# Optimization experiments

Hardware: AMD Instinct MI355X
Metric: run time of the kernel (lower is better)

## Reference

```python
import jax, jax.numpy as jnp
import numpy as np

IN_ = 64
FEATURE = 1024
BATCH = 256

def setup_inputs() -> dict:
    key = jax.random.key(0)
    kx, kw = jax.random.split(key)
    x = jax.random.normal(kx, (BATCH, IN_, FEATURE), dtype=jnp.float32)
    # W[i] corresponds to torch Linear weight of shape [out_features, in_features]
    # scaled like torch's default kaiming-uniform-ish init (bound = 1/sqrt(fan_in))
    bound = 1.0 / np.sqrt(FEATURE)
    W = jax.random.uniform(kw, (IN_, FEATURE, FEATURE), dtype=jnp.float32,
                           minval=-bound, maxval=bound)
    return {"x": x, "W": W}

def reference(x, W):
    # Per-position independent linear: out[b,i,o] = sum_f x[b,i,f] * W[i,o,f]
    # (torch Linear computes x @ W^T). Single batched GEMM via einsum.
    return jnp.einsum('bif,iof->bio', x, W)
```

## Files before the change

### kernel.cpp

```cpp
#include <hip/hip_runtime.h>
#include <hip/hip_bf16.h>

#define IN_CNT 64
#define FEAT   1024
#define BATCH  256

#define BM 256
#define BN 256
#define BK 64
#define KT (FEAT / BK)

typedef __attribute__((ext_vector_type(4))) float f32x4;
typedef __attribute__((ext_vector_type(4))) short bf16x4;
typedef __attribute__((ext_vector_type(8))) short bf16x8;

__device__ __forceinline__ short f2bf(float f) {
    __hip_bfloat16 h = __float2bfloat16(f);
    return __builtin_bit_cast(short, h);
}

__device__ __forceinline__ bf16x4 pack4(f32x4 a) {
    bf16x4 v;
    v[0] = f2bf(a[0]); v[1] = f2bf(a[1]); v[2] = f2bf(a[2]); v[3] = f2bf(a[3]);
    return v;
}

__device__ __forceinline__ void barrier_nodrain() {
    asm volatile("s_waitcnt lgkmcnt(0)" ::: "memory");
    __builtin_amdgcn_s_barrier();
    asm volatile("" ::: "memory");
}

__global__ __launch_bounds__(512, 2)
void split_linear_kernel(const float* __restrict__ x,
                         const float* __restrict__ W,
                         float* __restrict__ out)
{
    __shared__ __align__(16) short lds[65536];

    const int tid = threadIdx.x;

    const int bid = blockIdx.x;
    const int swz = ((bid & 7) << 5) | (bid >> 3);
    const int gi   = swz >> 2;
    const int ncol = (swz & 3) << 8;

    const int lane = tid & 63;
    const int wid  = tid >> 6;
    const int wm   = wid >> 2;
    const int wn   = wid & 3;
    const int lr   = lane & 15;
    const int lh   = lane >> 4;

    const int srow = wid * 4 + lh;
    const int gpos = lr;
    const float* Abase = x + ((size_t)srow * IN_CNT + gi) * FEAT + gpos * 4;
    const float* Bbase = W + ((size_t)gi * FEAT + ncol + srow) * FEAT + gpos * 4;

    f32x4 ra[8], rb[8];
    f32x4 acc[8][4];
#pragma unroll
    for (int m = 0; m < 8; ++m)
#pragma unroll
        for (int n = 0; n < 4; ++n)
            acc[m][n] = (f32x4){0.f, 0.f, 0.f, 0.f};

    auto LOADT = [&](int kt) {
#pragma unroll
        for (int i = 0; i < 8; ++i) {
            ra[i] = *(const f32x4*)(Abase + (size_t)kt * BK + (size_t)i * (32 * IN_CNT * FEAT));
            rb[i] = *(const f32x4*)(Bbase + (size_t)kt * BK + (size_t)i * (32 * FEAT));
        }
    };

    auto WRITET = [&](int b) {
        short* base = lds + b * 32768;
#pragma unroll
        for (int i = 0; i < 8; ++i) {
            const int r  = srow + i * 32;
            const int s8 = gpos ^ ((r & 7) << 1);
            *(bf16x4*)&base[r * 64 + s8 * 4]         = pack4(ra[i]);
            *(bf16x4*)&base[16384 + r * 64 + s8 * 4] = pack4(rb[i]);
        }
    };

    auto COMPUTE = [&](int b) {
        const short* baseA = lds + b * 32768;
        const short* baseB = baseA + 16384;
#pragma unroll
        for (int ks = 0; ks < 2; ++ks) {
            const int t = ks * 4 + lh;
            bf16x8 bf[4];
#pragma unroll
            for (int nf = 0; nf < 4; ++nf) {
                const int r = wn * 64 + nf * 16 + lr;
                bf[nf] = *(const bf16x8*)&baseB[r * 64 + ((t ^ (r & 7)) << 3)];
            }
#pragma unroll
            for (int mf = 0; mf < 8; ++mf) {
                const int r = wm * 128 + mf * 16 + lr;
                bf16x8 af = *(const bf16x8*)&baseA[r * 64 + ((t ^ (r & 7)) << 3)];
#pragma unroll
                for (int nf = 0; nf < 4; ++nf)
                    acc[mf][nf] = __builtin_amdgcn_mfma_f32_16x16x32_bf16(
                        af, bf[nf], acc[mf][nf], 0, 0, 0);
            }
        }
    };

    LOADT(0);
    WRITET(0);
    LOADT(1);
    barrier_nodrain();

    for (int kt = 0; kt < KT; ++kt) {
        const int b = kt & 1;
        if (kt + 1 < KT) WRITET(b ^ 1);
        if (kt + 2 < KT) LOADT(kt + 2);
        COMPUTE(b);
        barrier_nodrain();
    }

#define ELD 260
    float* elds = (float*)lds;
#pragma unroll
    for (int s = 0; s < 4; ++s) {
        barrier_nodrain();
        if (wm == (s >> 1)) {
            const int mfb = (s & 1) * 4;
#pragma unroll
            for (int f = 0; f < 4; ++f)
#pragma unroll
                for (int nf = 0; nf < 4; ++nf)
#pragma unroll
                    for (int j = 0; j < 4; ++j)
                        elds[(f * 16 + lh * 4 + j) * ELD + wn * 64 + nf * 16 + lr]
                            = acc[mfb + f][nf][j];
        }
        barrier_nodrain();
#pragma unroll
        for (int rr = 0; rr < 8; ++rr) {
            const int rowl = wid * 8 + rr;
            f32x4 v = *(const f32x4*)&elds[rowl * ELD + lane * 4];
            const int m = s * 64 + rowl;
            *(f32x4*)&out[((size_t)m * IN_CNT + gi) * FEAT + ncol + lane * 4] = v;
        }
    }
#undef ELD
}

extern "C" void kernel_launch(void* const* d_in, const int* in_sizes, int n_in,
                              void* d_out, int out_size, void* d_ws, size_t ws_size,
                              hipStream_t stream) {
    const float* x   = (const float*)d_in[0];
    const float* W   = (const float*)d_in[1];
    float*       out = (float*)d_out;

    dim3 grid(IN_CNT * (FEAT / BN));
    dim3 block(512);
    hipLaunchKernelGGL(split_linear_kernel, grid, block, 0, stream, x, W, out);
}
```

Measured before the change: 106.3 us.

## Stream fp32 tiles directly into LDS via global_load_lds, convert to bf16 at fragment read

Replaces the register-staged global load plus bf16 pack and LDS write with direct global-to-LDS DMA loads of fp32 data, using an XOR swizzle on the source column. The fp32-to-bf16 conversion moves to fragment-read time inside the compute loop. BK is halved to 32 so the double buffer fits in the same LDS, and synchronisation now relies on vmcnt waits. The aim is to free VGPRs and drop the VALU/LDS store traffic from the prologue of each k-step. In exchange, every wave now converts its own fragments, which repeats conversion work across waves and doubles the LDS read bytes, and there are twice as many barriers.

Measured after the change: 94.72 us. 10.9% less time.

```diff
diff --git a/kernel.cpp b/kernel.cpp
--- a/kernel.cpp
+++ b/kernel.cpp
@@ -7,11 +7,10 @@
 
 #define BM 256
 #define BN 256
-#define BK 64
+#define BK 32
 #define KT (FEAT / BK)
 
 typedef __attribute__((ext_vector_type(4))) float f32x4;
-typedef __attribute__((ext_vector_type(4))) short bf16x4;
 typedef __attribute__((ext_vector_type(8))) short bf16x8;
 
 __device__ __forceinline__ short f2bf(float f) {
@@ -19,16 +18,23 @@
     return __builtin_bit_cast(short, h);
 }
 
-__device__ __forceinline__ bf16x4 pack4(f32x4 a) {
-    bf16x4 v;
+__device__ __forceinline__ bf16x8 pack8(f32x4 a, f32x4 b) {
+    bf16x8 v;
     v[0] = f2bf(a[0]); v[1] = f2bf(a[1]); v[2] = f2bf(a[2]); v[3] = f2bf(a[3]);
+    v[4] = f2bf(b[0]); v[5] = f2bf(b[1]); v[6] = f2bf(b[2]); v[7] = f2bf(b[3]);
     return v;
 }
 
-__device__ __forceinline__ void barrier_nodrain() {
+__device__ __forceinline__ void barrier_lgkm() {
     asm volatile("s_waitcnt lgkmcnt(0)" ::: "memory");
     __builtin_amdgcn_s_barrier();
     asm volatile("" ::: "memory");
+}
+
+__device__ __forceinline__ void gload16(const float* g, float* l) {
+    __builtin_amdgcn_global_load_lds(
+        (const __attribute__((address_space(1))) void*)g,
+        (__attribute__((address_space(3))) void*)l, 16, 0, 0);
 }
 
 __global__ __launch_bounds__(512, 2)
@@ -36,7 +42,7 @@
                          const float* __restrict__ W,
                          float* __restrict__ out)
 {
-    __shared__ __align__(16) short lds[65536];
+    __shared__ __align__(16) float lds[32768];
 
     const int tid = threadIdx.x;
 
@@ -52,12 +58,11 @@
     const int lr   = lane & 15;
     const int lh   = lane >> 4;
 
-    const int srow = wid * 4 + lh;
-    const int gpos = lr;
-    const float* Abase = x + ((size_t)srow * IN_CNT + gi) * FEAT + gpos * 4;
-    const float* Bbase = W + ((size_t)gi * FEAT + ncol + srow) * FEAT + gpos * 4;
+    const int lrow = lane >> 3;
+    const int lgr  = (lane & 7) ^ lrow;
+    const float* Asrc = x + ((size_t)lrow * IN_CNT + gi) * FEAT + lgr * 4;
+    const float* Bsrc = W + ((size_t)gi * FEAT + ncol + lrow) * FEAT + lgr * 4;
 
-    f32x4 ra[8], rb[8];
     f32x4 acc[8][4];
 #pragma unroll
     for (int m = 0; m < 8; ++m)
@@ -65,67 +70,66 @@
         for (int n = 0; n < 4; ++n)
             acc[m][n] = (f32x4){0.f, 0.f, 0.f, 0.f};
 
-    auto LOADT = [&](int kt) {
+    auto ISSUE = [&](int kt, int b) {
+        float* base = lds + b * 16384;
+        const float* a0 = Asrc + (size_t)kt * BK;
+        const float* b0 = Bsrc + (size_t)kt * BK;
 #pragma unroll
-        for (int i = 0; i < 8; ++i) {
-            ra[i] = *(const f32x4*)(Abase + (size_t)kt * BK + (size_t)i * (32 * IN_CNT * FEAT));
-            rb[i] = *(const f32x4*)(Bbase + (size_t)kt * BK + (size_t)i * (32 * FEAT));
+        for (int i = 0; i < 4; ++i) {
+            const int c = wid * 4 + i;
+            gload16(a0 + (size_t)c * (8 * IN_CNT * FEAT), base + c * 256);
+            gload16(b0 + (size_t)c * (8 * FEAT),          base + 8192 + c * 256);
         }
     };
 
-    auto WRITET = [&](int b) {
-        short* base = lds + b * 32768;
+    const int sl0 = ((2 * lh)     ^ (lr & 7)) << 2;
+    const int sl1 = ((2 * lh + 1) ^ (lr & 7)) << 2;
+
+    auto COMPUTE = [&](int b) {
+        const float* bufA = lds + b * 16384;
+        const float* bufB = bufA + 8192;
+        bf16x8 bfr[4];
 #pragma unroll
-        for (int i = 0; i < 8; ++i) {
-            const int r  = srow + i * 32;
-            const int s8 = gpos ^ ((r & 7) << 1);
-            *(bf16x4*)&base[r * 64 + s8 * 4]         = pack4(ra[i]);
-            *(bf16x4*)&base[16384 + r * 64 + s8 * 4] = pack4(rb[i]);
+        for (int nf = 0; nf < 4; ++nf) {
+            const float* rp = bufB + (wn * 64 + nf * 16 + lr) * 32;
+            bfr[nf] = pack8(*(const f32x4*)(rp + sl0), *(const f32x4*)(rp + sl1));
+        }
+#pragma unroll
+        for (int mf = 0; mf < 8; ++mf) {
+            const float* rp = bufA + (wm * 128 + mf * 16 + lr) * 32;
+            bf16x8 af = pack8(*(const f32x4*)(rp + sl0), *(const f32x4*)(rp + sl1));
+#pragma unroll
+            for (int nf = 0; nf < 4; ++nf)
+                acc[mf][nf] = __builtin_amdgcn_mfma_f32_16x16x32_bf16(
+                    af, bfr[nf], acc[mf][nf], 0, 0, 0);
         }
     };
 
-    auto COMPUTE = [&](int b) {
-        const short* baseA = lds + b * 32768;
-        const short* baseB = baseA + 16384;
-#pragma unroll
-        for (int ks = 0; ks < 2; ++ks) {
-            const int t = ks * 4 + lh;
-            bf16x8 bf[4];
-#pragma unroll
-            for (int nf = 0; nf < 4; ++nf) {
-                const int r = wn * 64 + nf * 16 + lr;
-                bf[nf] = *(const bf16x8*)&baseB[r * 64 + ((t ^ (r & 7)) << 3)];
-            }
-#pragma unroll
-            for (int mf = 0; mf < 8; ++mf) {
-                const int r = wm * 128 + mf * 16 + lr;
-                bf16x8 af = *(const bf16x8*)&baseA[r * 64 + ((t ^ (r & 7)) << 3)];
-#pragma unroll
-                for (int nf = 0; nf < 4; ++nf)
-                    acc[mf][nf] = __builtin_amdgcn_mfma_f32_16x16x32_bf16(
-                        af, bf[nf], acc[mf][nf], 0, 0, 0);
-            }
+    ISSUE(0, 0);
+    ISSUE(1, 1);
+    asm volatile("s_waitcnt vmcnt(8)" ::: "memory");
+    __builtin_amdgcn_s_barrier();
+    asm volatile("" ::: "memory");
+
+    for (int k = 0; k < KT; ++k) {
+        const int b = k & 1;
+        COMPUTE(b);
+        barrier_lgkm();
+        if (k + 2 < KT) {
+            ISSUE(k + 2, b);
+            asm volatile("s_waitcnt vmcnt(8)" ::: "memory");
+        } else {
+            asm volatile("s_waitcnt vmcnt(0)" ::: "memory");
         }
-    };
-
-    LOADT(0);
-    WRITET(0);
-    LOADT(1);
-    barrier_nodrain();
-
-    for (int kt = 0; kt < KT; ++kt) {
-        const int b = kt & 1;
-        if (kt + 1 < KT) WRITET(b ^ 1);
-        if (kt + 2 < KT) LOADT(kt + 2);
-        COMPUTE(b);
-        barrier_nodrain();
+        __builtin_amdgcn_s_barrier();
+        asm volatile("" ::: "memory");
     }
 
 #define ELD 260
-    float* elds = (float*)lds;
+    float* elds = lds;
 #pragma unroll
     for (int s = 0; s < 4; ++s) {
-        barrier_nodrain();
+        barrier_lgkm();
         if (wm == (s >> 1)) {
             const int mfb = (s & 1) * 4;
 #pragma unroll
@@ -137,7 +141,7 @@
                         elds[(f * 16 + lh * 4 + j) * ELD + wn * 64 + nf * 16 + lr]
                             = acc[mfb + f][nf][j];
         }
-        barrier_nodrain();
+        barrier_lgkm();
 #pragma unroll
         for (int rr = 0; rr < 8; ++rr) {
             const int rowl = wid * 8 + rr;
```
